# Optimization experiments

Hardware: AMD Instinct MI355X
Metric: run time of the kernel (lower is better)

Reference implementation:

```python
import jax, jax.numpy as jnp
import numpy as np


def setup_inputs() -> dict:
    key = jax.random.key(0)
    k_x, k_w1, k_w2 = jax.random.split(key, 3)
    T, B, C, H, W = 32, 8, 64, 64, 64
    r = 1
    x = jax.random.normal(k_x, (T, B, C, H, W), dtype=jnp.float32)
    # torch nn.Linear weight layout: (out_features, in_features)
    w1 = jax.random.normal(k_w1, (T // r, T), dtype=jnp.float32) * (1.0 / np.sqrt(T))
    w2 = jax.random.normal(k_w2, (T, T // r), dtype=jnp.float32) * (1.0 / np.sqrt(T // r))
    return {"x": x, "w1": w1, "w2": w2}


def reference(x, w1, w2):
    # squeeze: global average pool over (C, H, W) per (t, b) -> (T, B)
    s = x.mean(axis=(2, 3, 4))
    # excite: MLP over the time axis, applied per batch element
    d = s.T                                   # (B, T)
    d = jax.nn.relu(d @ w1.T)                 # (B, T//r)
    d = jax.nn.sigmoid(d @ w2.T)              # (B, T)
    d = d.T                                   # (T, B)
    # broadcast scale
    return d[:, :, None, None, None] * x
```

## Files before the change

kernel.cpp:

```cpp
#include <hip/hip_runtime.h>
#include <math.h>

#define SLICE 262144
#define TBCNT 256

__global__ __launch_bounds__(1024) void se_sum_kernel(const float* __restrict__ x,
                                                      float* __restrict__ sums) {
    const int slice = blockIdx.x;
    const float4* xp = (const float4*)(x + (size_t)slice * SLICE);
    const int tid = threadIdx.x;

    float acc = 0.0f;
#pragma unroll
    for (int k = 0; k < SLICE / 4 / 1024; ++k) {
        float4 v = xp[tid + k * 1024];
        acc += (v.x + v.y) + (v.z + v.w);
    }

    for (int off = 32; off > 0; off >>= 1)
        acc += __shfl_down(acc, off, 64);

    __shared__ float lds[16];
    const int lane = tid & 63;
    const int wave = tid >> 6;
    if (lane == 0) lds[wave] = acc;
    __syncthreads();
    if (tid == 0) {
        float s = 0.0f;
#pragma unroll
        for (int w = 0; w < 16; ++w) s += lds[w];
        sums[slice] = s;
    }
}

__global__ __launch_bounds__(256) void se_mlp_kernel(const float* __restrict__ sums,
                                                     const float* __restrict__ w1,
                                                     const float* __restrict__ w2,
                                                     float* __restrict__ scale) {
    __shared__ float smean[TBCNT];
    __shared__ float h[8][32];
    const int tid = threadIdx.x;

    smean[tid] = sums[tid] * (1.0f / (float)SLICE);
    __syncthreads();

    const int b = tid >> 5;
    const int j = tid & 31;
    float a = 0.0f;
#pragma unroll
    for (int t = 0; t < 32; ++t) a += smean[t * 8 + b] * w1[j * 32 + t];
    h[b][j] = fmaxf(a, 0.0f);
    __syncthreads();

    const int t = tid & 31;
    float v = 0.0f;
#pragma unroll
    for (int jj = 0; jj < 32; ++jj) v += h[b][jj] * w2[t * 32 + jj];
    scale[t * 8 + b] = 1.0f / (1.0f + expf(-v));
}

__global__ __launch_bounds__(256) void se_scale_kernel(const float* __restrict__ x,
                                                       const float* __restrict__ scale,
                                                       float* __restrict__ out) {
    const size_t i4 = (size_t)blockIdx.x * 256 + threadIdx.x;
    const int tb = (int)(i4 >> 16);
    const float s = scale[tb];
    float4 v = ((const float4*)x)[i4];
    v.x *= s; v.y *= s; v.z *= s; v.w *= s;
    ((float4*)out)[i4] = v;
}

extern "C" void kernel_launch(void* const* d_in, const int* in_sizes, int n_in,
                              void* d_out, int out_size, void* d_ws, size_t ws_size,
                              hipStream_t stream) {
    const float* x  = (const float*)d_in[0];
    const float* w1 = (const float*)d_in[1];
    const float* w2 = (const float*)d_in[2];
    float* out = (float*)d_out;

    float* ws_sums  = (float*)d_ws;
    float* ws_scale = ws_sums + TBCNT;

    se_sum_kernel<<<TBCNT, 1024, 0, stream>>>(x, ws_sums);
    se_mlp_kernel<<<1, 256, 0, stream>>>(ws_sums, w1, w2, ws_scale);

    const size_t total4 = (size_t)TBCNT * SLICE / 4;
    se_scale_kernel<<<(int)(total4 / 256), 256, 0, stream>>>(x, ws_scale, out);
}
```

Before: 145.8 us.

## Split slice reduction across more blocks and use nontemporal stores in scale

The sum kernel moves from 256 blocks of 1024 threads to 2048 blocks of 256 threads. Each block writes a partial sum, and the MLP kernel adds up 8 partials per (t,b) slot. The aim is to fill more CUs during the reduction. The scale kernel now handles two float4 per thread and writes with nontemporal stores, which should cut launch and block overhead and keep output writes from evicting cached x. That matters because the scale pass re-reads x, which is 256MB and only partly fits in cache, so the cache benefit is uncertain.

```diff
diff --git a/kernel.cpp b/kernel.cpp
--- a/kernel.cpp
+++ b/kernel.cpp
@@ -3,37 +3,34 @@
 
 #define SLICE 262144
 #define TBCNT 256
+#define NPART 8
+#define SUMBLOCKS (TBCNT * NPART)
 
-__global__ __launch_bounds__(1024) void se_sum_kernel(const float* __restrict__ x,
-                                                      float* __restrict__ sums) {
-    const int slice = blockIdx.x;
-    const float4* xp = (const float4*)(x + (size_t)slice * SLICE);
+typedef float f32x4 __attribute__((ext_vector_type(4)));
+
+__global__ __launch_bounds__(256) void se_sum_kernel(const float* __restrict__ x,
+                                                     float* __restrict__ partial) {
+    const int bid = blockIdx.x;
     const int tid = threadIdx.x;
+    const f32x4* xp = (const f32x4*)x + (size_t)bid * 8192;
 
     float acc = 0.0f;
 #pragma unroll
-    for (int k = 0; k < SLICE / 4 / 1024; ++k) {
-        float4 v = xp[tid + k * 1024];
+    for (int k = 0; k < 32; ++k) {
+        f32x4 v = xp[tid + k * 256];
         acc += (v.x + v.y) + (v.z + v.w);
     }
 
     for (int off = 32; off > 0; off >>= 1)
         acc += __shfl_down(acc, off, 64);
 
-    __shared__ float lds[16];
-    const int lane = tid & 63;
-    const int wave = tid >> 6;
-    if (lane == 0) lds[wave] = acc;
+    __shared__ float lds[4];
+    if ((tid & 63) == 0) lds[tid >> 6] = acc;
     __syncthreads();
-    if (tid == 0) {
-        float s = 0.0f;
-#pragma unroll
-        for (int w = 0; w < 16; ++w) s += lds[w];
-        sums[slice] = s;
-    }
+    if (tid == 0) partial[bid] = (lds[0] + lds[1]) + (lds[2] + lds[3]);
 }
 
-__global__ __launch_bounds__(256) void se_mlp_kernel(const float* __restrict__ sums,
+__global__ __launch_bounds__(256) void se_mlp_kernel(const float* __restrict__ partial,
                                                      const float* __restrict__ w1,
                                                      const float* __restrict__ w2,
                                                      float* __restrict__ scale) {
@@ -41,7 +38,10 @@
     __shared__ float h[8][32];
     const int tid = threadIdx.x;
 
-    smean[tid] = sums[tid] * (1.0f / (float)SLICE);
+    float s = 0.0f;
+#pragma unroll
+    for (int k = 0; k < NPART; ++k) s += partial[tid * NPART + k];
+    smean[tid] = s * (1.0f / (float)SLICE);
     __syncthreads();
 
     const int b = tid >> 5;
@@ -62,12 +62,21 @@
 __global__ __launch_bounds__(256) void se_scale_kernel(const float* __restrict__ x,
                                                        const float* __restrict__ scale,
                                                        float* __restrict__ out) {
-    const size_t i4 = (size_t)blockIdx.x * 256 + threadIdx.x;
-    const int tb = (int)(i4 >> 16);
+    const size_t base = (size_t)blockIdx.x * 512;
+    const int tb = (int)(base >> 16);
     const float s = scale[tb];
-    float4 v = ((const float4*)x)[i4];
-    v.x *= s; v.y *= s; v.z *= s; v.w *= s;
-    ((float4*)out)[i4] = v;
+    const f32x4* xp = (const f32x4*)x;
+    f32x4* op = (f32x4*)out;
+
+    size_t i = base + threadIdx.x;
+    f32x4 v = xp[i];
+    v *= s;
+    __builtin_nontemporal_store(v, &op[i]);
+
+    size_t j = i + 256;
+    f32x4 u = xp[j];
+    u *= s;
+    __builtin_nontemporal_store(u, &op[j]);
 }
 
 extern "C" void kernel_launch(void* const* d_in, const int* in_sizes, int n_in,
@@ -78,12 +87,12 @@
     const float* w2 = (const float*)d_in[2];
     float* out = (float*)d_out;
 
-    float* ws_sums  = (float*)d_ws;
-    float* ws_scale = ws_sums + TBCNT;
+    float* ws_partial = (float*)d_ws;
+    float* ws_scale   = ws_partial + SUMBLOCKS;
 
-    se_sum_kernel<<<TBCNT, 1024, 0, stream>>>(x, ws_sums);
-    se_mlp_kernel<<<1, 256, 0, stream>>>(ws_sums, w1, w2, ws_scale);
+    se_sum_kernel<<<SUMBLOCKS, 256, 0, stream>>>(x, ws_partial);
+    se_mlp_kernel<<<1, 256, 0, stream>>>(ws_partial, w1, w2, ws_scale);
 
     const size_t total4 = (size_t)TBCNT * SLICE / 4;
-    se_scale_kernel<<<(int)(total4 / 256), 256, 0, stream>>>(x, ws_scale, out);
+    se_scale_kernel<<<(int)(total4 / 512), 256, 0, stream>>>(x, ws_scale, out);
 }
```

After: 122.6 us. -15.9%, faster.

## Fuse SE reduce, MLP and scale into one cooperative kernel with on-chip bf16 hold

Applied to the files above, without the earlier changes.

Replaces the three kernels with a single cooperative-grid kernel. Each block sums its slice while keeping most of it on chip as packed bf16, split between registers and LDS. After a grid-wide sync, each block computes its own MLP scale and writes the scaled output from the held copy, re-reading only a small tail from global memory. This removes the second full read of x and two kernel launches. The cost is lossy bf16 rounding of the outputs, heavy register and LDS pressure, and reliance on all 256 blocks being co-resident.

```diff
diff --git a/kernel.cpp b/kernel.cpp
--- a/kernel.cpp
+++ b/kernel.cpp
@@ -1,73 +1,118 @@
 #include <hip/hip_runtime.h>
+#include <hip/hip_cooperative_groups.h>
 #include <math.h>
 
+#define TBCNT 256
 #define SLICE 262144
-#define TBCNT 256
+#define THREADS 512
+#define K_TOTAL 128
+#define K_REG 100
+#define K_LDS 15
 
-__global__ __launch_bounds__(1024) void se_sum_kernel(const float* __restrict__ x,
-                                                      float* __restrict__ sums) {
-    const int slice = blockIdx.x;
-    const float4* xp = (const float4*)(x + (size_t)slice * SLICE);
+typedef float f32x4 __attribute__((ext_vector_type(4)));
+
+__device__ __forceinline__ unsigned pack2(float a, float b) {
+    unsigned ua = __float_as_uint(a), ub = __float_as_uint(b);
+    ua = (ua + 0x7FFFu + ((ua >> 16) & 1u)) >> 16;
+    ub = (ub + 0x7FFFu + ((ub >> 16) & 1u)) & 0xFFFF0000u;
+    return ua | ub;
+}
+
+__device__ __forceinline__ f32x4 unpack4(unsigned lo, unsigned hi, float s) {
+    f32x4 v;
+    v.x = __uint_as_float(lo << 16) * s;
+    v.y = __uint_as_float(lo & 0xFFFF0000u) * s;
+    v.z = __uint_as_float(hi << 16) * s;
+    v.w = __uint_as_float(hi & 0xFFFF0000u) * s;
+    return v;
+}
+
+__global__ __launch_bounds__(THREADS, 2) void se_fused(
+        const float* __restrict__ x, const float* __restrict__ w1,
+        const float* __restrict__ w2, float* __restrict__ out,
+        float* __restrict__ sums) {
+    __shared__ unsigned uhold[K_LDS * 2 * THREADS];
+    __shared__ float red[8];
+    __shared__ float hsh[32];
+    __shared__ float scsh;
+
+    const int bid = blockIdx.x;
     const int tid = threadIdx.x;
+    const f32x4* xp = (const f32x4*)x + (size_t)bid * (SLICE / 4);
 
+    unsigned hr[2 * K_REG];
     float acc = 0.0f;
 #pragma unroll
-    for (int k = 0; k < SLICE / 4 / 1024; ++k) {
-        float4 v = xp[tid + k * 1024];
+    for (int k = 0; k < K_REG; ++k) {
+        f32x4 v = xp[k * THREADS + tid];
+        acc += (v.x + v.y) + (v.z + v.w);
+        hr[2 * k]     = pack2(v.x, v.y);
+        hr[2 * k + 1] = pack2(v.z, v.w);
+    }
+#pragma unroll
+    for (int k = 0; k < K_LDS; ++k) {
+        f32x4 v = xp[(K_REG + k) * THREADS + tid];
+        acc += (v.x + v.y) + (v.z + v.w);
+        uhold[(2 * k) * THREADS + tid]     = pack2(v.x, v.y);
+        uhold[(2 * k + 1) * THREADS + tid] = pack2(v.z, v.w);
+    }
+#pragma unroll
+    for (int k = K_REG + K_LDS; k < K_TOTAL; ++k) {
+        f32x4 v = xp[k * THREADS + tid];
         acc += (v.x + v.y) + (v.z + v.w);
     }
 
     for (int off = 32; off > 0; off >>= 1)
         acc += __shfl_down(acc, off, 64);
-
-    __shared__ float lds[16];
-    const int lane = tid & 63;
-    const int wave = tid >> 6;
-    if (lane == 0) lds[wave] = acc;
+    if ((tid & 63) == 0) red[tid >> 6] = acc;
     __syncthreads();
     if (tid == 0) {
         float s = 0.0f;
 #pragma unroll
-        for (int w = 0; w < 16; ++w) s += lds[w];
-        sums[slice] = s;
+        for (int w = 0; w < 8; ++w) s += red[w];
+        sums[bid] = s;
     }
-}
+    __threadfence();
 
-__global__ __launch_bounds__(256) void se_mlp_kernel(const float* __restrict__ sums,
-                                                     const float* __restrict__ w1,
-                                                     const float* __restrict__ w2,
-                                                     float* __restrict__ scale) {
-    __shared__ float smean[TBCNT];
-    __shared__ float h[8][32];
-    const int tid = threadIdx.x;
+    cooperative_groups::this_grid().sync();
 
-    smean[tid] = sums[tid] * (1.0f / (float)SLICE);
+    const int b = bid & 7, tself = bid >> 3;
+    if (tid < 32) {
+        float a = 0.0f;
+#pragma unroll
+        for (int t = 0; t < 32; ++t)
+            a += (sums[t * 8 + b] * (1.0f / (float)SLICE)) * w1[tid * 32 + t];
+        hsh[tid] = fmaxf(a, 0.0f);
+    }
     __syncthreads();
+    if (tid == 0) {
+        float vv = 0.0f;
+#pragma unroll
+        for (int j = 0; j < 32; ++j) vv += hsh[j] * w2[tself * 32 + j];
+        scsh = 1.0f / (1.0f + expf(-vv));
+    }
+    __syncthreads();
+    const float s = scsh;
 
-    const int b = tid >> 5;
-    const int j = tid & 31;
-    float a = 0.0f;
+    f32x4* op = (f32x4*)out + (size_t)bid * (SLICE / 4);
 #pragma unroll
-    for (int t = 0; t < 32; ++t) a += smean[t * 8 + b] * w1[j * 32 + t];
-    h[b][j] = fmaxf(a, 0.0f);
-    __syncthreads();
-
-    const int t = tid & 31;
-    float v = 0.0f;
+    for (int k = 0; k < K_REG; ++k) {
+        f32x4 v = unpack4(hr[2 * k], hr[2 * k + 1], s);
+        __builtin_nontemporal_store(v, &op[k * THREADS + tid]);
+    }
 #pragma unroll
-    for (int jj = 0; jj < 32; ++jj) v += h[b][jj] * w2[t * 32 + jj];
-    scale[t * 8 + b] = 1.0f / (1.0f + expf(-v));
-}
-
-__global__ __launch_bounds__(256) void se_scale_kernel(const float* __restrict__ x,
-                                                       const float* __restrict__ scale,
-                                                       float* __restrict__ out) {
-    const size_t i4 = (size_t)blockIdx.x * 256 + threadIdx.x;
-    const int tb = (int)(i4 >> 16);
-    const float s = scale[tb];
-    float4 v = ((const float4*)x)[i4];
-    v.x *= s; v.y *= s; v.z *= s; v.w *= s;
-    ((float4*)out)[i4] = v;
+    for (int k = 0; k < K_LDS; ++k) {
+        unsigned lo = uhold[(2 * k) * THREADS + tid];
+        unsigned hi = uhold[(2 * k + 1) * THREADS + tid];
+        f32x4 v = unpack4(lo, hi, s);
+        __builtin_nontemporal_store(v, &op[(K_REG + k) * THREADS + tid]);
+    }
+#pragma unroll
+    for (int k = K_REG + K_LDS; k < K_TOTAL; ++k) {
+        f32x4 v = xp[k * THREADS + tid];
+        v *= s;
+        __builtin_nontemporal_store(v, &op[k * THREADS + tid]);
+    }
 }
 
 extern "C" void kernel_launch(void* const* d_in, const int* in_sizes, int n_in,
@@ -76,14 +121,10 @@
     const float* x  = (const float*)d_in[0];
     const float* w1 = (const float*)d_in[1];
     const float* w2 = (const float*)d_in[2];
-    float* out = (float*)d_out;
+    float* out  = (float*)d_out;
+    float* sums = (float*)d_ws;
 
-    float* ws_sums  = (float*)d_ws;
-    float* ws_scale = ws_sums + TBCNT;
-
-    se_sum_kernel<<<TBCNT, 1024, 0, stream>>>(x, ws_sums);
-    se_mlp_kernel<<<1, 256, 0, stream>>>(ws_sums, w1, w2, ws_scale);
-
-    const size_t total4 = (size_t)TBCNT * SLICE / 4;
-    se_scale_kernel<<<(int)(total4 / 256), 256, 0, stream>>>(x, ws_scale, out);
+    void* args[] = {(void*)&x, (void*)&w1, (void*)&w2, (void*)&out, (void*)&sums};
+    hipLaunchCooperativeKernel((const void*)se_fused, dim3(TBCNT), dim3(THREADS),
+                               args, 0, stream);
 }
```

Result: slower. 286.8 us (+96.7%).
